# Performance work log

Hardware: AMD Instinct MI355X
Metric: run time of the kernel (lower is better)

The kernel has to match this reference:

```python
import jax, jax.numpy as jnp
import numpy as np

INF = 1e38  # matches torch module's INF = 1e+38


def setup_inputs() -> dict:
    key = jax.random.key(0)
    k1, k2, k3 = jax.random.split(key, 3)
    n_len, batch, dim = 2048, 4, 512
    # scale query so QK^T logits don't fully saturate the softmax
    query = jax.random.normal(k1, (n_len, batch, dim), dtype=jnp.float32) * 0.05
    W_in = jax.random.normal(k2, (dim, dim), dtype=jnp.float32) * (1.0 / np.sqrt(dim))
    W_out = jax.random.normal(k3, (dim, 2 * dim), dtype=jnp.float32) * (1.0 / np.sqrt(2 * dim))
    return {"query": query, "W_in": W_in, "W_out": W_out}


def reference(query, W_in, W_out):
    # query: [n_len, batch, dim]; torch .t() swaps first two dims -> [batch, n_len, dim]
    q = jnp.transpose(query, (1, 0, 2))
    b, n, d = q.shape
    # attention_type == 'general': linear_in (no bias), y = x @ W^T
    q = jnp.einsum('bnd,ed->bne', q, W_in)
    # scores: [b, n, n]
    scores = jnp.einsum('bnd,bmd->bnm', q, q)
    # mask = triu(ones) INCLUDING diagonal -> set to -INF (row 0 fully masked)
    mask = jnp.triu(jnp.ones((n, n), dtype=bool))
    scores = jnp.where(mask[None, :, :], -INF, scores)
    weights = jax.nn.softmax(scores, axis=-1)  # row 0 becomes uniform (all -INF)
    # manual zero-out of row 0 of the attention weights
    weights = weights.at[:, 0, :].set(0.0)
    mix = jnp.einsum('bnm,bmd->bnd', weights, q)
    combined = jnp.concatenate([mix, q], axis=-1)  # [b, n, 2d]
    out = jnp.einsum('bnk,dk->bnd', combined, W_out)  # linear_out, no bias
    out = jax.nn.selu(out)
    # final .t() -> [n_len, batch, dim]
    return jnp.transpose(out, (1, 0, 2)), weights
```

## Files before the change

kernel.cpp:

```cpp
#include <hip/hip_runtime.h>
#include <hip/hip_bf16.h>

typedef unsigned short u16;
typedef unsigned int u32;

#define BATCH 4
#define NLEN 2048
#define DIM 512
#define LDSK 40
#define LDSB 72

typedef __attribute__((ext_vector_type(8))) __bf16 bf16x8;
typedef __attribute__((ext_vector_type(4))) float f32x4;

__device__ __forceinline__ u16 f32_to_bf16(float f) {
  union { float f; u32 u; } v; v.f = f;
  u32 u = v.u;
  return (u16)((u + 0x7FFFu + ((u >> 16) & 1u)) >> 16);
}
__device__ __forceinline__ u32 pk2(float lo, float hi) {
  return (u32)f32_to_bf16(lo) | ((u32)f32_to_bf16(hi) << 16);
}
__device__ __forceinline__ void stage8_f32(u16* dst, const float* src) {
  float4 a = *(const float4*)src;
  float4 b = *(const float4*)(src + 4);
  uint4 o;
  o.x = pk2(a.x, a.y); o.y = pk2(a.z, a.w);
  o.z = pk2(b.x, b.y); o.w = pk2(b.z, b.w);
  *(uint4*)dst = o;
}
__device__ __forceinline__ void stage16_f32(u16* dst, const float* src) {
  stage8_f32(dst, src); stage8_f32(dst + 8, src + 8);
}
__device__ __forceinline__ void stage8_bf16(u16* dst, const u16* src) {
  *(uint4*)dst = *(const uint4*)src;
}
__device__ __forceinline__ void stage16_bf16(u16* dst, const u16* src) {
  *(uint4*)dst = *(const uint4*)src;
  *(uint4*)(dst + 8) = *(const uint4*)(src + 8);
}
__device__ __forceinline__ void stage8_sum(u16* dst, const u16* s0, const u16* s1,
                                           const u16* s2, int cnt) {
  uint4 a = *(const uint4*)s0;
  u32 wa[4] = {a.x, a.y, a.z, a.w};
  float v[8];
#pragma unroll
  for (int i = 0; i < 4; ++i) {
    v[2 * i] = __uint_as_float(wa[i] << 16);
    v[2 * i + 1] = __uint_as_float(wa[i] & 0xffff0000u);
  }
  if (cnt > 1) {
    uint4 bq = *(const uint4*)s1;
    u32 wb[4] = {bq.x, bq.y, bq.z, bq.w};
#pragma unroll
    for (int i = 0; i < 4; ++i) {
      v[2 * i] += __uint_as_float(wb[i] << 16);
      v[2 * i + 1] += __uint_as_float(wb[i] & 0xffff0000u);
    }
  }
  if (cnt > 2) {
    uint4 cq = *(const uint4*)s2;
    u32 wc[4] = {cq.x, cq.y, cq.z, cq.w};
#pragma unroll
    for (int i = 0; i < 4; ++i) {
      v[2 * i] += __uint_as_float(wc[i] << 16);
      v[2 * i + 1] += __uint_as_float(wc[i] & 0xffff0000u);
    }
  }
  uint4 o;
  o.x = pk2(v[0], v[1]); o.y = pk2(v[2], v[3]);
  o.z = pk2(v[4], v[5]); o.w = pk2(v[6], v[7]);
  *(uint4*)dst = o;
}

template <int MR, int NR>
__device__ __forceinline__ void mma_tile(const u16* As, const u16* Bs, f32x4 acc[MR][NR],
                                         int wm, int wn, int lr, int lk) {
  bf16x8 af[MR], bfr[NR];
#pragma unroll
  for (int m = 0; m < MR; ++m)
    af[m] = *(const bf16x8*)(As + (wm + m * 16 + lr) * LDSK + lk);
#pragma unroll
  for (int n = 0; n < NR; ++n)
    bfr[n] = *(const bf16x8*)(Bs + (wn + n * 16 + lr) * LDSK + lk);
#pragma unroll
  for (int m = 0; m < MR; ++m)
#pragma unroll
    for (int n = 0; n < NR; ++n)
      acc[m][n] = __builtin_amdgcn_mfma_f32_16x16x32_bf16(af[m], bfr[n], acc[m][n], 0, 0, 0);
}

__global__ __launch_bounds__(256) void k_qproj(const float* __restrict__ query,
                                               const float* __restrict__ W_in,
                                               u16* __restrict__ qp, u16* __restrict__ qt) {
  __shared__ u16 As[64 * LDSK];
  __shared__ u16 Bs[128 * LDSK];
  __shared__ u16 tbuf[128][72];
  const int t = threadIdx.x;
  const int lane = t & 63, wid = t >> 6;
  const int wm = (wid >> 1) * 32, wn = (wid & 1) * 64;
  const int lr = lane & 15, lk = (lane >> 4) * 8;
  const int trow4 = t >> 2, tseg = (t & 3) * 8;
  const int trow2 = t >> 1, thalf = (t & 1) * 16;
  const int rbase = blockIdx.y * 64;
  const int cbase = blockIdx.x * 128;
  const int rg = rbase + trow4;
  const int bb = rg >> 11, nn = rg & 2047;
  const float* aRow = query + (size_t)(nn * BATCH + bb) * DIM + tseg;
  const float* bRow = W_in + (size_t)(cbase + trow2) * DIM + thalf;
  f32x4 acc[2][4] = {};
  for (int k0 = 0; k0 < DIM; k0 += 32) {
    stage8_f32(As + trow4 * LDSK + tseg, aRow + k0);
    stage16_f32(Bs + trow2 * LDSK + thalf, bRow + k0);
    __syncthreads();
    mma_tile<2, 4>(As, Bs, acc, wm, wn, lr, lk);
    __syncthreads();
  }
#pragma unroll
  for (int m = 0; m < 2; ++m)
#pragma unroll
    for (int n = 0; n < 4; ++n)
#pragma unroll
      for (int j = 0; j < 4; ++j) {
        int rl = wm + m * 16 + (lane >> 4) * 4 + j;
        int cl = wn + n * 16 + lr;
        u16 v = f32_to_bf16(acc[m][n][j]);
        qp[(size_t)(rbase + rl) * DIM + cbase + cl] = v;
        tbuf[cl][rl] = v;
      }
  __syncthreads();
  const int bb0 = rbase >> 11, nbase = rbase & 2047;
#pragma unroll
  for (int i = 0; i < 4; ++i) {
    int idx = t + i * 256;
    int dl = idx >> 3, c = idx & 7;
    uint4 v = *(const uint4*)&tbuf[dl][c * 8];
    *(uint4*)(qt + (size_t)(bb0 * DIM + cbase + dl) * NLEN + nbase + c * 8) = v;
  }
}

__global__ __launch_bounds__(256) void k_scores(const u16* __restrict__ qp,
                                                u16* __restrict__ swf) {
  const int mt = blockIdx.x;
  const int nt = blockIdx.y;
  const int b = blockIdx.z;
  if (mt > (nt >> 1)) return;
  __shared__ u16 As[64 * LDSK];
  __shared__ u16 Bs[128 * LDSK];
  const int t = threadIdx.x;
  const int lane = t & 63, wid = t >> 6;
  const int wm = (wid >> 1) * 32, wn = (wid & 1) * 64;
  const int lr = lane & 15, lk = (lane >> 4) * 8;
  const int trow4 = t >> 2, tseg = (t & 3) * 8;
  const int trow2 = t >> 1, thalf = (t & 1) * 16;
  const u16* aRow = qp + (size_t)(b * NLEN + nt * 64 + trow4) * DIM + tseg;
  const u16* bRow = qp + (size_t)(b * NLEN + mt * 128 + trow2) * DIM + thalf;
  f32x4 acc[2][4] = {};
  for (int k0 = 0; k0 < DIM; k0 += 32) {
    stage8_bf16(As + trow4 * LDSK + tseg, aRow + k0);
    stage16_bf16(Bs + trow2 * LDSK + thalf, bRow + k0);
    __syncthreads();
    mma_tile<2, 4>(As, Bs, acc, wm, wn, lr, lk);
    __syncthreads();
  }
  const int NT = nt >> 1;
  u16* wtile = swf + ((size_t)(b * 136 + NT * (NT + 1) / 2 + mt) << 14);
  const int rowoff = (nt & 1) * 64;
#pragma unroll
  for (int m = 0; m < 2; ++m)
#pragma unroll
    for (int n = 0; n < 4; ++n)
#pragma unroll
      for (int j = 0; j < 4; ++j) {
        int rl = wm + m * 16 + (lane >> 4) * 4 + j;
        int cl = wn + n * 16 + lr;
        wtile[(rowoff + rl) * 128 + cl] = f32_to_bf16(acc[m][n][j]);
      }
}

__global__ __launch_bounds__(256) void k_softmax(u16* __restrict__ swf, float* __restrict__ w) {
  const int n = blockIdx.x, b = blockIdx.y;
  const int t = threadIdx.x;
  float* wrow = w + ((size_t)b * NLEN + n) * NLEN;
  const int nt = n >> 7;
  const size_t tb = ((size_t)(b * 136 + nt * (nt + 1) / 2) << 14) + ((size_t)(n & 127) << 7);
  __shared__ float srow[NLEN];
  __shared__ float red[4];
  if (n == 0) {
    for (int i = t; i < NLEN / 4; i += 256) ((float4*)wrow)[i] = float4{0, 0, 0, 0};
    if (t < 16) ((uint4*)(swf + tb))[t] = uint4{0, 0, 0, 0};
    return;
  }
  const int lane = t & 63, wid = t >> 6;
  const int nchunk = (nt + 1) * 16;
  float mx = -1e38f;
  for (int idx = t; idx < nchunk; idx += 256) {
    const int mt = idx >> 4, c = idx & 15;
    uint4 rv = *(const uint4*)(swf + tb + ((size_t)mt << 14) + c * 8);
    int m0 = mt * 128 + c * 8;
    u32 wds[4] = {rv.x, rv.y, rv.z, rv.w};
#pragma unroll
    for (int wi = 0; wi < 4; ++wi) {
      float v0 = __uint_as_float(wds[wi] << 16);
      float v1 = __uint_as_float(wds[wi] & 0xffff0000u);
      int m = m0 + wi * 2;
      srow[m] = v0; srow[m + 1] = v1;
      if (m < n) mx = fmaxf(mx, v0);
      if (m + 1 < n) mx = fmaxf(mx, v1);
    }
  }
#pragma unroll
  for (int off = 32; off; off >>= 1) mx = fmaxf(mx, __shfl_xor(mx, off));
  if (lane == 0) red[wid] = mx;
  __syncthreads();
  mx = fmaxf(fmaxf(red[0], red[1]), fmaxf(red[2], red[3]));
  float sum = 0.f;
  for (int m = t; m < n; m += 256) {
    float e = __expf(srow[m] - mx);
    srow[m] = e;
    sum += e;
  }
#pragma unroll
  for (int off = 32; off; off >>= 1) sum += __shfl_xor(sum, off);
  __syncthreads();
  if (lane == 0) red[wid] = sum;
  __syncthreads();
  float inv = 1.0f / (red[0] + red[1] + red[2] + red[3]);
  {
    int m0 = t * 8;
    float vals[8];
#pragma unroll
    for (int e = 0; e < 8; ++e) { int m = m0 + e; vals[e] = (m < n) ? srow[m] * inv : 0.f; }
    ((float4*)wrow)[t * 2] = float4{vals[0], vals[1], vals[2], vals[3]};
    ((float4*)wrow)[t * 2 + 1] = float4{vals[4], vals[5], vals[6], vals[7]};
  }
  for (int idx = t; idx < nchunk; idx += 256) {
    const int mt = idx >> 4, c = idx & 15;
    int m0 = mt * 128 + c * 8;
    u32 wo[4];
#pragma unroll
    for (int wi = 0; wi < 4; ++wi) {
      int m = m0 + wi * 2;
      float v0 = (m < n) ? srow[m] * inv : 0.f;
      float v1 = (m + 1 < n) ? srow[m + 1] * inv : 0.f;
      wo[wi] = (u32)f32_to_bf16(v0) | ((u32)f32_to_bf16(v1) << 16);
    }
    *(uint4*)(swf + tb + ((size_t)mt << 14) + c * 8) = uint4{wo[0], wo[1], wo[2], wo[3]};
  }
}

__global__ __launch_bounds__(256) void k_mix(const u16* __restrict__ swf,
                                             const u16* __restrict__ qt,
                                             u16* __restrict__ mixp) {
  const size_t PSZ = (size_t)BATCH * NLEN * DIM;
  const int bid = blockIdx.x;
  const int b = bid / 132;
  const int rem = bid % 132;
  const int dt = rem / 33;
  const int j = rem % 33;
  int nt, cp, P;
  if (j < 18) { nt = 15 - j / 3; cp = j % 3; P = 3; }
  else if (j < 28) { int jj = j - 18; nt = 9 - (jj >> 1); cp = jj & 1; P = 2; }
  else { nt = 32 - j; cp = 0; P = 1; }
  const int S = nt + 1;
  const int ks = cp * S / P, ke = (cp + 1) * S / P;
  __shared__ u16 As[128 * LDSK];
  __shared__ u16 Bs[128 * LDSK];
  const int t = threadIdx.x;
  const int lane = t & 63, wid = t >> 6;
  const int wm = (wid >> 1) * 64, wn = (wid & 1) * 64;
  const int lr = lane & 15, lk = (lane >> 4) * 8;
  const int trow2 = t >> 1, thalf = (t & 1) * 16;
  const size_t tribase = (size_t)(b * 136 + nt * (nt + 1) / 2) << 14;
  const u16* bRow = qt + (size_t)(b * DIM + dt * 128 + trow2) * NLEN + thalf;
  f32x4 acc[4][4] = {};
  for (int kstep = ks * 4; kstep < ke * 4; ++kstep) {
    const int k0 = kstep * 32;
    const int mt = k0 >> 7;
    const u16* aRow = swf + tribase + ((size_t)mt << 14) + trow2 * 128 + (k0 & 127) + thalf;
    stage16_bf16(As + trow2 * LDSK + thalf, aRow);
    stage16_bf16(Bs + trow2 * LDSK + thalf, bRow + k0);
    __syncthreads();
    mma_tile<4, 4>(As, Bs, acc, wm, wn, lr, lk);
    __syncthreads();
  }
  u16* dst = mixp + (size_t)cp * PSZ;
#pragma unroll
  for (int m = 0; m < 4; ++m)
#pragma unroll
    for (int n = 0; n < 4; ++n)
#pragma unroll
      for (int j2 = 0; j2 < 4; ++j2) {
        int row = nt * 128 + wm + m * 16 + (lane >> 4) * 4 + j2;
        int col = dt * 128 + wn + n * 16 + lr;
        dst[(size_t)(b * NLEN + row) * DIM + col] = f32_to_bf16(acc[m][n][j2]);
      }
}

__global__ __launch_bounds__(256) void k_fin(const u16* __restrict__ mixp,
                                             u16* __restrict__ amix,
                                             const float* __restrict__ W_out,
                                             u16* __restrict__ wob) {
  const size_t PSZ = (size_t)BATCH * NLEN * DIM;
  const int bid = blockIdx.x;
  const int t = threadIdx.x;
  if (bid < 512) {
#pragma unroll
    for (int i = 0; i < 4; ++i) {
      int g = i * 131072 + bid * 256 + t;
      int row = g >> 6, chunk = g & 63;
      int nt = (row & 2047) >> 7;
      int cnt = (nt >= 10) ? 3 : ((nt >= 5) ? 2 : 1);
      size_t off = (size_t)row * DIM + chunk * 8;
      stage8_sum(amix + off, mixp + off, mixp + PSZ + off, mixp + 2 * PSZ + off, cnt);
    }
  } else {
    int g = (bid - 512) * 256 + t;
    stage8_f32(wob + (size_t)g * 8, W_out + (size_t)g * 8);
  }
}

__global__ __launch_bounds__(256) void k_out(const u16* __restrict__ amix,
                                             const u16* __restrict__ qp,
                                             const u16* __restrict__ wob,
                                             float* __restrict__ out) {
  __shared__ u16 As[128 * LDSB];
  __shared__ u16 Bs[64 * LDSB];
  const int et = blockIdx.x;
  const int rt = blockIdx.y;
  const int t = threadIdx.x;
  const int lane = t & 63, wid = t >> 6;
  const int wm = (wid >> 1) * 64, wn = (wid & 1) * 32;
  const int lr = lane & 15, lk = (lane >> 4) * 8;
  const int rbase = rt * 128;
  const int ar = t >> 3, ac = (t & 7) * 8;
  const int br = t >> 2, bc = (t & 3) * 16;
  const u16* aMix = amix + (size_t)rbase * DIM;
  const u16* aQ = qp + (size_t)rbase * DIM;
  const u16* bW = wob + (size_t)(et * 64 + br) * (2 * DIM) + bc;
  f32x4 acc[4][2] = {};
  for (int k0 = 0; k0 < 2 * DIM; k0 += 64) {
    const u16* asrc = (k0 < DIM) ? (aMix + k0) : (aQ + (k0 - DIM));
#pragma unroll
    for (int i = 0; i < 4; ++i)
      *(uint4*)(As + (ar + i * 32) * LDSB + ac) =
          *(const uint4*)(asrc + (size_t)(ar + i * 32) * DIM + ac);
    *(uint4*)(Bs + br * LDSB + bc) = *(const uint4*)(bW + k0);
    *(uint4*)(Bs + br * LDSB + bc + 8) = *(const uint4*)(bW + k0 + 8);
    __syncthreads();
#pragma unroll
    for (int kk = 0; kk < 64; kk += 32) {
      bf16x8 af[4], bfr[2];
#pragma unroll
      for (int m = 0; m < 4; ++m)
        af[m] = *(const bf16x8*)(As + (wm + m * 16 + lr) * LDSB + kk + lk);
#pragma unroll
      for (int n = 0; n < 2; ++n)
        bfr[n] = *(const bf16x8*)(Bs + (wn + n * 16 + lr) * LDSB + kk + lk);
#pragma unroll
      for (int m = 0; m < 4; ++m)
#pragma unroll
        for (int n = 0; n < 2; ++n)
          acc[m][n] = __builtin_amdgcn_mfma_f32_16x16x32_bf16(af[m], bfr[n], acc[m][n], 0, 0, 0);
    }
    __syncthreads();
  }
  const float sc = 1.0507009873554805f;
  const float al = 1.6732632423543772f;
#pragma unroll
  for (int m = 0; m < 4; ++m)
#pragma unroll
    for (int n = 0; n < 2; ++n)
#pragma unroll
      for (int j = 0; j < 4; ++j) {
        int row = rbase + wm + m * 16 + (lane >> 4) * 4 + j;
        int col = et * 64 + wn + n * 16 + lr;
        int b2 = row >> 11, n2 = row & 2047;
        float v = acc[m][n][j];
        v = (v > 0.f) ? sc * v : sc * al * (__expf(v) - 1.f);
        out[(size_t)(n2 * BATCH + b2) * DIM + col] = v;
      }
}

extern "C" void kernel_launch(void* const* d_in, const int* in_sizes, int n_in,
                              void* d_out, int out_size, void* d_ws, size_t ws_size,
                              hipStream_t stream) {
  const float* query = (const float*)d_in[0];
  const float* W_in = (const float*)d_in[1];
  const float* W_out = (const float*)d_in[2];
  float* out0 = (float*)d_out;
  float* w = out0 + (size_t)NLEN * BATCH * DIM;

  const size_t PSZ = (size_t)BATCH * NLEN * DIM;
  u16* qp = (u16*)d_ws;
  u16* qt = qp + PSZ;
  u16* mixp = qt + PSZ;
  u16* swf = mixp + 3 * PSZ;
  u16* wob = swf + (size_t)BATCH * 136 * 16384;
  u16* amix = qt;

  dim3 blk(256);
  k_qproj<<<dim3(DIM / 128, (BATCH * NLEN) / 64), blk, 0, stream>>>(query, W_in, qp, qt);
  k_scores<<<dim3(16, 32, BATCH), blk, 0, stream>>>(qp, swf);
  k_softmax<<<dim3(NLEN, BATCH), blk, 0, stream>>>(swf, w);
  k_mix<<<dim3(528), blk, 0, stream>>>(swf, qt, mixp);
  k_fin<<<dim3(768), blk, 0, stream>>>(mixp, amix, W_out, wob);
  k_out<<<dim3(8, 64), blk, 0, stream>>>(amix, qp, wob, out0);
}
```

Baseline: 139.5 us.

## Replace split-K mix partials with row-split tiles, drop reduction kernel

The mix GEMM no longer splits long K ranges into partial sums that a separate kernel adds up. Instead, the longest row tiles are split into two 64-row halves that each run the full K range and write bf16 results straight to the final mix buffer. The W_out bf16 conversion moves into extra blocks of the softmax kernel, which removes one launch and the round trip of the partial buffers. In exchange, the half-row tiles use smaller MFMA tiles and reload the B operand twice, and load balance across the 448 blocks may be worse.

Result: no change. 140.2 us (+0.5%).

```diff
diff --git a/kernel.cpp b/kernel.cpp
--- a/kernel.cpp
+++ b/kernel.cpp
@@ -38,39 +38,6 @@
 __device__ __forceinline__ void stage16_bf16(u16* dst, const u16* src) {
   *(uint4*)dst = *(const uint4*)src;
   *(uint4*)(dst + 8) = *(const uint4*)(src + 8);
-}
-__device__ __forceinline__ void stage8_sum(u16* dst, const u16* s0, const u16* s1,
-                                           const u16* s2, int cnt) {
-  uint4 a = *(const uint4*)s0;
-  u32 wa[4] = {a.x, a.y, a.z, a.w};
-  float v[8];
-#pragma unroll
-  for (int i = 0; i < 4; ++i) {
-    v[2 * i] = __uint_as_float(wa[i] << 16);
-    v[2 * i + 1] = __uint_as_float(wa[i] & 0xffff0000u);
-  }
-  if (cnt > 1) {
-    uint4 bq = *(const uint4*)s1;
-    u32 wb[4] = {bq.x, bq.y, bq.z, bq.w};
-#pragma unroll
-    for (int i = 0; i < 4; ++i) {
-      v[2 * i] += __uint_as_float(wb[i] << 16);
-      v[2 * i + 1] += __uint_as_float(wb[i] & 0xffff0000u);
-    }
-  }
-  if (cnt > 2) {
-    uint4 cq = *(const uint4*)s2;
-    u32 wc[4] = {cq.x, cq.y, cq.z, cq.w};
-#pragma unroll
-    for (int i = 0; i < 4; ++i) {
-      v[2 * i] += __uint_as_float(wc[i] << 16);
-      v[2 * i + 1] += __uint_as_float(wc[i] & 0xffff0000u);
-    }
-  }
-  uint4 o;
-  o.x = pk2(v[0], v[1]); o.y = pk2(v[2], v[3]);
-  o.z = pk2(v[4], v[5]); o.w = pk2(v[6], v[7]);
-  *(uint4*)dst = o;
 }
 
 template <int MR, int NR>
@@ -178,9 +145,20 @@
       }
 }
 
-__global__ __launch_bounds__(256) void k_softmax(u16* __restrict__ swf, float* __restrict__ w) {
+__global__ __launch_bounds__(256) void k_softmax(u16* __restrict__ swf, float* __restrict__ w,
+                                                 const float* __restrict__ W_out,
+                                                 u16* __restrict__ wob) {
   const int n = blockIdx.x, b = blockIdx.y;
   const int t = threadIdx.x;
+  if (n >= NLEN) {
+    int g = ((n - NLEN) * 4 + b) * 256 + t;
+#pragma unroll
+    for (int i = 0; i < 4; ++i) {
+      int e = g * 32 + i * 8;
+      stage8_f32(wob + e, W_out + e);
+    }
+    return;
+  }
   float* wrow = w + ((size_t)b * NLEN + n) * NLEN;
   const int nt = n >> 7;
   const size_t tb = ((size_t)(b * 136 + nt * (nt + 1) / 2) << 14) + ((size_t)(n & 127) << 7);
@@ -249,74 +227,64 @@
   }
 }
 
+template <int ROWS>
+__device__ __forceinline__ void mix_body(u16* As, u16* Bs,
+                                         const u16* __restrict__ swf,
+                                         const u16* __restrict__ qt,
+                                         u16* __restrict__ amix,
+                                         int b, int dt, int nt, int seg) {
+  constexpr int MR = (ROWS == 128) ? 4 : 2;
+  constexpr int NR = 4;
+  const int t = threadIdx.x;
+  const int lane = t & 63, wid = t >> 6;
+  const int wm = (wid >> 1) * (ROWS / 2), wn = (wid & 1) * 64;
+  const int lr = lane & 15, lk = (lane >> 4) * 8;
+  const int trow2 = t >> 1, thalf = (t & 1) * 16;
+  const int ar = (ROWS == 128) ? (t >> 1) : (t >> 2);
+  const int ac = (ROWS == 128) ? ((t & 1) * 16) : ((t & 3) * 8);
+  const size_t tribase = (size_t)(b * 136 + nt * (nt + 1) / 2) << 14;
+  const int rowloc = seg * ROWS;
+  const u16* bRow = qt + (size_t)(b * DIM + dt * 128 + trow2) * NLEN + thalf;
+  f32x4 acc[MR][NR] = {};
+  const int nsteps = (nt + 1) * 4;
+  for (int kstep = 0; kstep < nsteps; ++kstep) {
+    const int k0 = kstep * 32;
+    const int mt = k0 >> 7;
+    const u16* aSrc = swf + tribase + ((size_t)mt << 14) + (rowloc + ar) * 128 + (k0 & 127) + ac;
+    if (ROWS == 128) stage16_bf16(As + ar * LDSK + ac, aSrc);
+    else stage8_bf16(As + ar * LDSK + ac, aSrc);
+    stage16_bf16(Bs + trow2 * LDSK + thalf, bRow + k0);
+    __syncthreads();
+    mma_tile<MR, NR>(As, Bs, acc, wm, wn, lr, lk);
+    __syncthreads();
+  }
+#pragma unroll
+  for (int m = 0; m < MR; ++m)
+#pragma unroll
+    for (int n = 0; n < NR; ++n)
+#pragma unroll
+      for (int j2 = 0; j2 < 4; ++j2) {
+        int row = nt * 128 + rowloc + wm + m * 16 + (lane >> 4) * 4 + j2;
+        int col = dt * 128 + wn + n * 16 + lr;
+        amix[(size_t)(b * NLEN + row) * DIM + col] = f32_to_bf16(acc[m][n][j2]);
+      }
+}
+
 __global__ __launch_bounds__(256) void k_mix(const u16* __restrict__ swf,
                                              const u16* __restrict__ qt,
-                                             u16* __restrict__ mixp) {
-  const size_t PSZ = (size_t)BATCH * NLEN * DIM;
-  const int bid = blockIdx.x;
-  const int b = bid / 132;
-  const int rem = bid % 132;
-  const int dt = rem / 33;
-  const int j = rem % 33;
-  int nt, cp, P;
-  if (j < 18) { nt = 15 - j / 3; cp = j % 3; P = 3; }
-  else if (j < 28) { int jj = j - 18; nt = 9 - (jj >> 1); cp = jj & 1; P = 2; }
-  else { nt = 32 - j; cp = 0; P = 1; }
-  const int S = nt + 1;
-  const int ks = cp * S / P, ke = (cp + 1) * S / P;
+                                             u16* __restrict__ amix) {
   __shared__ u16 As[128 * LDSK];
   __shared__ u16 Bs[128 * LDSK];
-  const int t = threadIdx.x;
-  const int lane = t & 63, wid = t >> 6;
-  const int wm = (wid >> 1) * 64, wn = (wid & 1) * 64;
-  const int lr = lane & 15, lk = (lane >> 4) * 8;
-  const int trow2 = t >> 1, thalf = (t & 1) * 16;
-  const size_t tribase = (size_t)(b * 136 + nt * (nt + 1) / 2) << 14;
-  const u16* bRow = qt + (size_t)(b * DIM + dt * 128 + trow2) * NLEN + thalf;
-  f32x4 acc[4][4] = {};
-  for (int kstep = ks * 4; kstep < ke * 4; ++kstep) {
-    const int k0 = kstep * 32;
-    const int mt = k0 >> 7;
-    const u16* aRow = swf + tribase + ((size_t)mt << 14) + trow2 * 128 + (k0 & 127) + thalf;
-    stage16_bf16(As + trow2 * LDSK + thalf, aRow);
-    stage16_bf16(Bs + trow2 * LDSK + thalf, bRow + k0);
-    __syncthreads();
-    mma_tile<4, 4>(As, Bs, acc, wm, wn, lr, lk);
-    __syncthreads();
-  }
-  u16* dst = mixp + (size_t)cp * PSZ;
-#pragma unroll
-  for (int m = 0; m < 4; ++m)
-#pragma unroll
-    for (int n = 0; n < 4; ++n)
-#pragma unroll
-      for (int j2 = 0; j2 < 4; ++j2) {
-        int row = nt * 128 + wm + m * 16 + (lane >> 4) * 4 + j2;
-        int col = dt * 128 + wn + n * 16 + lr;
-        dst[(size_t)(b * NLEN + row) * DIM + col] = f32_to_bf16(acc[m][n][j2]);
-      }
-}
-
-__global__ __launch_bounds__(256) void k_fin(const u16* __restrict__ mixp,
-                                             u16* __restrict__ amix,
-                                             const float* __restrict__ W_out,
-                                             u16* __restrict__ wob) {
-  const size_t PSZ = (size_t)BATCH * NLEN * DIM;
   const int bid = blockIdx.x;
-  const int t = threadIdx.x;
-  if (bid < 512) {
-#pragma unroll
-    for (int i = 0; i < 4; ++i) {
-      int g = i * 131072 + bid * 256 + t;
-      int row = g >> 6, chunk = g & 63;
-      int nt = (row & 2047) >> 7;
-      int cnt = (nt >= 10) ? 3 : ((nt >= 5) ? 2 : 1);
-      size_t off = (size_t)row * DIM + chunk * 8;
-      stage8_sum(amix + off, mixp + off, mixp + PSZ + off, mixp + 2 * PSZ + off, cnt);
-    }
+  const int j = bid >> 4;
+  const int bdt = bid & 15;
+  const int b = bdt >> 2, dt = bdt & 3;
+  if (j < 24) {
+    const int nt = 15 - (j >> 1), seg = j & 1;
+    mix_body<64>(As, Bs, swf, qt, amix, b, dt, nt, seg);
   } else {
-    int g = (bid - 512) * 256 + t;
-    stage8_f32(wob + (size_t)g * 8, W_out + (size_t)g * 8);
+    const int nt = 27 - j;
+    mix_body<128>(As, Bs, swf, qt, amix, b, dt, nt, 0);
   }
 }
 
@@ -394,16 +362,14 @@
   const size_t PSZ = (size_t)BATCH * NLEN * DIM;
   u16* qp = (u16*)d_ws;
   u16* qt = qp + PSZ;
-  u16* mixp = qt + PSZ;
-  u16* swf = mixp + 3 * PSZ;
+  u16* amix = qt + PSZ;
+  u16* swf = amix + PSZ;
   u16* wob = swf + (size_t)BATCH * 136 * 16384;
-  u16* amix = qt;
 
   dim3 blk(256);
   k_qproj<<<dim3(DIM / 128, (BATCH * NLEN) / 64), blk, 0, stream>>>(query, W_in, qp, qt);
   k_scores<<<dim3(16, 32, BATCH), blk, 0, stream>>>(qp, swf);
-  k_softmax<<<dim3(NLEN, BATCH), blk, 0, stream>>>(swf, w);
-  k_mix<<<dim3(528), blk, 0, stream>>>(swf, qt, mixp);
-  k_fin<<<dim3(768), blk, 0, stream>>>(mixp, amix, W_out, wob);
+  k_softmax<<<dim3(NLEN + 16, BATCH), blk, 0, stream>>>(swf, w, W_out, wob);
+  k_mix<<<dim3(448), blk, 0, stream>>>(swf, qt, amix);
   k_out<<<dim3(8, 64), blk, 0, stream>>>(amix, qp, wob, out0);
 }
```
